# Performance work log

Measured on AMD Instinct MI355X. Metric: run time of the kernel, lower is better.

The kernel has to match this reference:

```python
import jax, jax.numpy as jnp
import numpy as np

DECAY = 0.95     # importance_decay
BUDGET = 1.0     # attention_budget
TOP_K = 10       # recall top_k used by get_context_embedding
EPS = 1e-8


def _gelu(x):
    # torch nn.GELU default = exact erf variant
    return jax.nn.gelu(x, approximate=False)


def setup_inputs() -> dict:
    key = jax.random.key(0)
    ks = jax.random.split(key, 8)
    B, N, D, H = 4096, 100, 4096, 128
    query = jax.random.normal(ks[0], (B, D), dtype=jnp.float32)
    seg_emb = jax.random.normal(ks[1], (N, D), dtype=jnp.float32)
    positions = jnp.arange(N, dtype=jnp.int32)
    s1 = 1.0 / np.sqrt(D)
    s2 = 1.0 / np.sqrt(H)
    iw1 = jax.random.normal(ks[2], (D, H), dtype=jnp.float32) * s1
    ib1 = jnp.zeros((H,), dtype=jnp.float32)
    iw2 = jax.random.normal(ks[3], (H, 1), dtype=jnp.float32) * s2
    ib2 = jnp.zeros((1,), dtype=jnp.float32)
    rw1 = jax.random.normal(ks[4], (2 * D, H), dtype=jnp.float32) * (1.0 / np.sqrt(2 * D))
    rb1 = jnp.zeros((H,), dtype=jnp.float32)
    rw2 = jax.random.normal(ks[5], (H, 1), dtype=jnp.float32) * s2
    rb2 = jnp.zeros((1,), dtype=jnp.float32)
    return {"query": query, "seg_emb": seg_emb, "positions": positions,
            "iw1": iw1, "ib1": ib1, "iw2": iw2, "ib2": ib2,
            "rw1": rw1, "rb1": rb1, "rw2": rw2, "rb2": rb2}


def reference(query, seg_emb, positions, iw1, ib1, iw2, ib2, rw1, rb1, rw2, rb2):
    # query: [B, D], seg_emb: [N, D]
    B, D = query.shape
    N = seg_emb.shape[0]

    # importance_scorer per segment: Linear->GELU->Linear->Sigmoid, [N]
    importance = jax.nn.sigmoid(_gelu(seg_emb @ iw1 + ib1) @ iw2 + ib2)[:, 0]

    # relevance_scorer on concat([query, seg]); split rw1 to avoid [B,N,2D] concat
    qh = query @ rw1[:D]            # [B, H]
    sh = seg_emb @ rw1[D:]          # [N, H]
    h = _gelu(qh[:, None, :] + sh[None, :, :] + rb1)   # [B, N, H]
    rel = jax.nn.sigmoid(jnp.einsum('bnh,ho->bn', h, rw2) + rb2[0])  # [B, N]

    # recall score: importance * relevance * (0.5 + 0.5 * decay^(N - pos - 1))
    pos_factor = DECAY ** (N - positions.astype(jnp.float32) - 1.0)  # [N]
    score = importance[None, :] * rel * (0.5 + 0.5 * pos_factor[None, :])

    _, topi = jax.lax.top_k(score, TOP_K)               # [B, K]

    sel_rel = jnp.take_along_axis(rel, topi, axis=1)    # [B, K]
    sel_imp = importance[topi]                          # [B, K]
    w = sel_imp * sel_rel
    w = w / (jnp.sum(w, axis=-1, keepdims=True) + EPS) * BUDGET

    sel_emb = seg_emb[topi]                             # [B, K, D]
    context = jnp.einsum('bk,bkd->bd', w, sel_emb)      # [B, D]
    return query + context
```

## Files before the change

kernel.cpp:

```cpp
#include <hip/hip_runtime.h>
#include <math.h>

#define DDIM 4096
#define NSEG 100
#define HDIM 128
#define BROWS 4096
#define TOPK 10
#define KSLICES 8

typedef __attribute__((ext_vector_type(8))) short bf16x8;
typedef __attribute__((ext_vector_type(4))) float f32x4;
typedef __attribute__((ext_vector_type(2))) float f32x2;

__device__ __forceinline__ void gl16(const void* g, void* l) {
    __builtin_amdgcn_global_load_lds(
        (const __attribute__((address_space(1))) unsigned int*)g,
        (__attribute__((address_space(3))) unsigned int*)l,
        16, 0, 0);
}

__device__ __forceinline__ float gelu_f(float x) {
    float u  = x * 0.70710678118654752440f;
    float au = fminf(fabsf(u), 3.9f);
    float t  = __builtin_amdgcn_rcpf(fmaf(0.3275911f, au, 1.0f));
    float p  = fmaf(fmaf(fmaf(fmaf(1.061405429f, t, -1.453152027f), t,
                              1.421413741f), t, -0.284496736f), t, 0.254829592f) * t;
    float e  = __expf(-au * au);
    float er = fmaf(-p, e, 1.0f);
    er = copysignf(er, u);
    return 0.5f * x * (1.0f + er);
}

__device__ __forceinline__ f32x2 gelu2(f32x2 x) {
    f32x2 u  = x * 0.70710678118654752440f;
    f32x2 au = __builtin_elementwise_min(__builtin_elementwise_abs(u), (f32x2)(3.9f));
    f32x2 den = __builtin_elementwise_fma((f32x2)(0.3275911f), au, (f32x2)(1.0f));
    f32x2 t;
    t.x = __builtin_amdgcn_rcpf(den.x);
    t.y = __builtin_amdgcn_rcpf(den.y);
    f32x2 p = __builtin_elementwise_fma(
                __builtin_elementwise_fma(
                  __builtin_elementwise_fma(
                    __builtin_elementwise_fma((f32x2)(1.061405429f), t, (f32x2)(-1.453152027f)),
                    t, (f32x2)(1.421413741f)),
                  t, (f32x2)(-0.284496736f)),
                t, (f32x2)(0.254829592f)) * t;
    f32x2 e;
    e.x = __expf(-au.x * au.x);
    e.y = __expf(-au.y * au.y);
    f32x2 er = __builtin_elementwise_fma(-p, e, (f32x2)(1.0f));
    er.x = copysignf(er.x, u.x);
    er.y = copysignf(er.y, u.y);
    return 0.5f * x * ((f32x2)(1.0f) + er);
}

__device__ __forceinline__ void split8(const float4& a, const float4& b,
                                       bf16x8& hi, bf16x8& lo) {
    float v[8] = {a.x, a.y, a.z, a.w, b.x, b.y, b.z, b.w};
    uint hw[4], lw[4];
    #pragma unroll
    for (int j = 0; j < 4; ++j) {
        uint u0 = __float_as_uint(v[2 * j]);
        uint u1 = __float_as_uint(v[2 * j + 1]);
        hw[j] = (u0 >> 16) | (u1 & 0xffff0000u);
        float r0 = v[2 * j]     - __uint_as_float(u0 & 0xffff0000u);
        float r1 = v[2 * j + 1] - __uint_as_float(u1 & 0xffff0000u);
        lw[j] = (__float_as_uint(r0) >> 16) | (__float_as_uint(r1) & 0xffff0000u);
    }
    uint4 h = make_uint4(hw[0], hw[1], hw[2], hw[3]);
    uint4 l = make_uint4(lw[0], lw[1], lw[2], lw[3]);
    hi = __builtin_bit_cast(bf16x8, h);
    lo = __builtin_bit_cast(bf16x8, l);
}

__global__ void k_front(const float* __restrict__ seg,
                        const float* __restrict__ iw1,
                        const float* __restrict__ rw1,
                        float* __restrict__ segp,
                        unsigned char* __restrict__ btI) {
    __shared__ __align__(16) float shf[32 * 129];
    int bid = blockIdx.x, tid = threadIdx.x;
    if (bid < 1600) {
        float (*segT)[5] = reinterpret_cast<float (*)[5]>(shf);
        int ng = bid % 25;
        int ks = (bid / 25) * 64;
        {
            int k = tid & 63, j = tid >> 6;
            segT[k][j] = seg[(size_t)(ng * 4 + j) * DDIM + ks + k];
        }
        __syncthreads();
        int col = tid;
        float a0 = 0.f, a1 = 0.f, a2 = 0.f, a3 = 0.f;
        const float* w = (col < HDIM) ? (iw1 + col)
                                      : (rw1 + (size_t)DDIM * HDIM + (col - HDIM));
        #pragma unroll 8
        for (int k = 0; k < 64; ++k) {
            float wv = w[(size_t)(ks + k) * HDIM];
            a0 = fmaf(segT[k][0], wv, a0);
            a1 = fmaf(segT[k][1], wv, a1);
            a2 = fmaf(segT[k][2], wv, a2);
            a3 = fmaf(segT[k][3], wv, a3);
        }
        float* outp = segp + (size_t)(bid / 25) * (NSEG * 256) + (size_t)(ng * 4) * 256 + col;
        outp[0] = a0; outp[256] = a1; outp[512] = a2; outp[768] = a3;
    } else {
        float (*tile)[129] = reinterpret_cast<float (*)[129]>(shf);
        int c = bid - 1600;
        #pragma unroll
        for (int i = 0; i < 4; ++i) {
            int e = i * 1024 + tid * 4;
            int k = e >> 7, n = e & 127;
            *reinterpret_cast<float4*>(&tile[k][n]) =
                *reinterpret_cast<const float4*>(rw1 + (size_t)(c * 32 + k) * HDIM + n);
        }
        __syncthreads();
        unsigned char* img = btI + (size_t)c * 16384;
        #pragma unroll
        for (int uu = 0; uu < 2; ++uu) {
            int U = tid * 2 + uu;
            int col = U >> 2;
            int u = U & 3;
            int Z = (col * 64 + u * 16) ^ ((col & 7) << 4);
            uint hw[4], lw[4];
            #pragma unroll
            for (int j = 0; j < 4; ++j) {
                float x0 = tile[u * 8 + 2 * j][col];
                float x1 = tile[u * 8 + 2 * j + 1][col];
                uint u0 = __float_as_uint(x0), u1 = __float_as_uint(x1);
                hw[j] = (u0 >> 16) | (u1 & 0xffff0000u);
                float r0 = x0 - __uint_as_float(u0 & 0xffff0000u);
                float r1 = x1 - __uint_as_float(u1 & 0xffff0000u);
                lw[j] = (__float_as_uint(r0) >> 16) | (__float_as_uint(r1) & 0xffff0000u);
            }
            *reinterpret_cast<uint4*>(img + Z)        = make_uint4(hw[0], hw[1], hw[2], hw[3]);
            *reinterpret_cast<uint4*>(img + 8192 + Z) = make_uint4(lw[0], lw[1], lw[2], lw[3]);
        }
    }
}

__global__ __launch_bounds__(256)
void k_mid(const float* __restrict__ query,
           const unsigned char* __restrict__ btI,
           float* __restrict__ qhp,
           const float* __restrict__ segp,
           const int* __restrict__ positions,
           const float* __restrict__ ib1,
           const float* __restrict__ iw2,
           const float* __restrict__ ib2,
           const float* __restrict__ rb1,
           float* __restrict__ shwT, float* __restrict__ impA,
           float* __restrict__ cA) {
    __shared__ __align__(16) char lds[49152];
    int bid = blockIdx.x, tid = threadIdx.x;
    if (bid < 512) {
        float  (*Ab)[2048] = reinterpret_cast<float (*)[2048]>(lds);
        ushort (*Bb)[8192] = reinterpret_cast<ushort (*)[8192]>(lds + 16384);
        int lane = tid & 63, w = tid >> 6;
        int cl = lane & 15, rg = lane >> 4;
        int wm = w >> 1, wn = w & 1;
        int m0 = (bid & 63) * 64;
        int ky = bid >> 6;
        int k0 = ky * 512;

        const float* aSrc0;
        const float* aSrc1;
        {
            int X0 = w * 2048 + lane * 16;
            int r0_ = X0 >> 7, kb0 = (X0 & 127) ^ ((r0_ & 7) << 4);
            aSrc0 = query + (size_t)(m0 + r0_) * DDIM + k0 + (kb0 >> 2);
            int X1 = X0 + 1024;
            int r1_ = X1 >> 7, kb1 = (X1 & 127) ^ ((r1_ & 7) << 4);
            aSrc1 = query + (size_t)(m0 + r1_) * DDIM + k0 + (kb1 >> 2);
        }
        const unsigned char* bSrc = btI + (size_t)(ky * 16) * 16384 + w * 4096 + lane * 16;

        f32x4 acc[2][4];
        #pragma unroll
        for (int mi = 0; mi < 2; ++mi)
            #pragma unroll
            for (int nf = 0; nf < 4; ++nf) acc[mi][nf] = (f32x4)0.f;

        {
            char* ad = (char*)&Ab[0][0] + w * 2048;
            char* bd = (char*)&Bb[0][0] + w * 4096;
            gl16(aSrc0, ad);
            gl16(aSrc1, ad + 1024);
            #pragma unroll
            for (int j = 0; j < 4; ++j) gl16(bSrc + j * 1024, bd + j * 1024);
        }
        __syncthreads();

        #pragma unroll 2
        for (int t = 0; t < 16; ++t) {
            int cur = t & 1;
            if (t < 15) {
                char* ad = (char*)&Ab[cur ^ 1][0] + w * 2048;
                char* bd = (char*)&Bb[cur ^ 1][0] + w * 4096;
                gl16(aSrc0 + (t + 1) * 32, ad);
                gl16(aSrc1 + (t + 1) * 32, ad + 1024);
                const unsigned char* bs = bSrc + (size_t)(t + 1) * 16384;
                #pragma unroll
                for (int j = 0; j < 4; ++j) gl16(bs + j * 1024, bd + j * 1024);
            }
            bf16x8 ah[2], al[2];
            #pragma unroll
            for (int mi = 0; mi < 2; ++mi) {
                int row = wm * 32 + mi * 16 + cl;
                int sw = (row & 7) << 4;
                int Sb = row * 128 + rg * 32;
                float4 f0 = *reinterpret_cast<const float4*>((const char*)&Ab[cur][0] + (Sb ^ sw));
                float4 f1 = *reinterpret_cast<const float4*>((const char*)&Ab[cur][0] + ((Sb + 16) ^ sw));
                split8(f0, f1, ah[mi], al[mi]);
            }
            #pragma unroll
            for (int nf = 0; nf < 4; ++nf) {
                int col = wn * 64 + nf * 16 + cl;
                int Z = (col * 64 + rg * 16) ^ ((col & 7) << 4);
                bf16x8 bh = *reinterpret_cast<const bf16x8*>((const char*)&Bb[cur][0] + Z);
                bf16x8 bl = *reinterpret_cast<const bf16x8*>((const char*)&Bb[cur][0] + 8192 + Z);
                #pragma unroll
                for (int mi = 0; mi < 2; ++mi) {
                    acc[mi][nf] = __builtin_amdgcn_mfma_f32_16x16x32_bf16(ah[mi], bh, acc[mi][nf], 0, 0, 0);
                    acc[mi][nf] = __builtin_amdgcn_mfma_f32_16x16x32_bf16(al[mi], bh, acc[mi][nf], 0, 0, 0);
                    acc[mi][nf] = __builtin_amdgcn_mfma_f32_16x16x32_bf16(ah[mi], bl, acc[mi][nf], 0, 0, 0);
                }
            }
            __syncthreads();
        }

        float* op = qhp + (size_t)ky * (BROWS * HDIM);
        #pragma unroll
        for (int mi = 0; mi < 2; ++mi) {
            int rowb = m0 + wm * 32 + mi * 16 + rg * 4;
            #pragma unroll
            for (int nf = 0; nf < 4; ++nf) {
                int col = wn * 64 + nf * 16 + cl;
                #pragma unroll
                for (int r = 0; r < 4; ++r)
                    op[(size_t)(rowb + r) * HDIM + col] = acc[mi][nf][r];
            }
        }
    } else {
        float* red = reinterpret_cast<float*>(lds);
        int n = bid - 512;
        float v = 0.f;
        #pragma unroll
        for (int s = 0; s < 64; ++s)
            v += segp[(size_t)s * (NSEG * 256) + (size_t)n * 256 + tid];
        if (tid < HDIM) {
            red[tid] = gelu_f(v + ib1[tid]) * iw2[tid];
        } else {
            shwT[(size_t)(tid - HDIM) * NSEG + n] = v + rb1[tid - HDIM];
        }
        __syncthreads();
        if (tid == 0) {
            float s = 0.f;
            for (int j = 0; j < HDIM; ++j) s += red[j];
            float imp = 1.f / (1.f + expf(-(s + ib2[0])));
            float pf = powf(0.95f, (float)NSEG - (float)positions[n] - 1.0f);
            impA[n] = imp;
            cA[n] = imp * (0.5f + 0.5f * pf);
        }
    }
}

__global__ __launch_bounds__(256)
void k_rel(const float* __restrict__ qhp,
           const float* __restrict__ shwT,
           const float* __restrict__ rw2,
           const float* __restrict__ rb2,
           const float* __restrict__ impA,
           const float* __restrict__ cA,
           int* __restrict__ idxA,
           float* __restrict__ wnA) {
    __shared__ float qs[4][HDIM];
    __shared__ float scL[4][128], wiL[4][128];
    int tid = threadIdx.x;
    int b0 = blockIdx.x * 4;

    #pragma unroll
    for (int i = 0; i < 2; ++i) {
        int idx = tid + i * 256;
        int r = idx >> 7, h = idx & 127;
        size_t o = (size_t)(b0 + r) * HDIM + h;
        float v = qhp[o];
        #pragma unroll
        for (int s = 1; s < KSLICES; ++s)
            v += qhp[(size_t)s * (BROWS * HDIM) + o];
        qs[r][h] = v;
    }
    __syncthreads();

    int w = tid >> 6, lane = tid & 63;
    int r = w;
    bool act = (lane < 50);
    int n0 = act ? (2 * lane) : 98;
    f32x2 a0_ = (f32x2)(0.f), a1_ = (f32x2)(0.f);
    f32x2 a2_ = (f32x2)(0.f), a3_ = (f32x2)(0.f);
    #pragma unroll 2
    for (int h = 0; h < 32; ++h) {
        f32x2 sA = *reinterpret_cast<const f32x2*>(&shwT[(h)      * NSEG + n0]);
        f32x2 sB = *reinterpret_cast<const f32x2*>(&shwT[(h + 32) * NSEG + n0]);
        f32x2 sC = *reinterpret_cast<const f32x2*>(&shwT[(h + 64) * NSEG + n0]);
        f32x2 sD = *reinterpret_cast<const f32x2*>(&shwT[(h + 96) * NSEG + n0]);
        a0_ = __builtin_elementwise_fma(gelu2(qs[r][h]      + sA), (f32x2)(rw2[h]),      a0_);
        a1_ = __builtin_elementwise_fma(gelu2(qs[r][h + 32] + sB), (f32x2)(rw2[h + 32]), a1_);
        a2_ = __builtin_elementwise_fma(gelu2(qs[r][h + 64] + sC), (f32x2)(rw2[h + 64]), a2_);
        a3_ = __builtin_elementwise_fma(gelu2(qs[r][h + 96] + sD), (f32x2)(rw2[h + 96]), a3_);
    }
    f32x2 acc = (a0_ + a1_) + (a2_ + a3_);
    if (act) {
        float rb2f = rb2[0];
        float rel0 = 1.f / (1.f + expf(-(acc.x + rb2f)));
        float rel1 = 1.f / (1.f + expf(-(acc.y + rb2f)));
        scL[r][n0]     = cA[n0] * rel0;      wiL[r][n0]     = impA[n0] * rel0;
        scL[r][n0 + 1] = cA[n0 + 1] * rel1;  wiL[r][n0 + 1] = impA[n0 + 1] * rel1;
    }
    __syncthreads();

    {
        int rr = w;
        float s1 = scL[rr][lane];
        float w1 = wiL[rr][lane];
        int i2 = lane + 64;
        float s2 = (i2 < NSEG) ? scL[rr][i2] : -1e30f;
        float w2 = (i2 < NSEG) ? wiL[rr][i2] : 0.f;

        float wv[TOPK]; int idxv[TOPK]; float wsum = 0.f;
        #pragma unroll
        for (int k = 0; k < TOPK; ++k) {
            float s; int i;
            if (s2 > s1) { s = s2; i = i2; } else { s = s1; i = lane; }
            #pragma unroll
            for (int off = 1; off < 64; off <<= 1) {
                float os = __shfl_xor(s, off);
                int oi = __shfl_xor(i, off);
                if (os > s || (os == s && oi < i)) { s = os; i = oi; }
            }
            float wi = __shfl((i < 64) ? w1 : w2, i & 63);
            idxv[k] = i; wv[k] = wi; wsum += wi;
            if (i == lane) s1 = -1e30f;
            if (i == i2)   s2 = -1e30f;
        }
        if (lane == 0) {
            int b = b0 + rr;
            float denom = wsum + 1e-8f;
            #pragma unroll
            for (int k = 0; k < TOPK; ++k) {
                idxA[b * TOPK + k] = idxv[k];
                wnA[b * TOPK + k]  = wv[k] / denom;
            }
        }
    }
}

__global__ void k_gather(const float* __restrict__ query,
                         const float* __restrict__ seg,
                         const int* __restrict__ idxA,
                         const float* __restrict__ wnA,
                         float* __restrict__ out) {
    int b = blockIdx.x, tid = threadIdx.x;
    const int*   ip = idxA + b * TOPK;
    const float* wp = wnA  + b * TOPK;
    float wn[TOPK]; const float* srow[TOPK];
    #pragma unroll
    for (int k = 0; k < TOPK; ++k) {
        wn[k]   = wp[k];
        srow[k] = seg + (size_t)ip[k] * DDIM;
    }
    const float* qrow = query + (size_t)b * DDIM;
    float* orow = out + (size_t)b * DDIM;

    float4 q[4];
    #pragma unroll
    for (int c = 0; c < 4; ++c)
        q[c] = *reinterpret_cast<const float4*>(qrow + c * 1024 + tid * 4);
    #pragma unroll
    for (int k = 0; k < TOPK; ++k) {
        float4 s[4];
        #pragma unroll
        for (int c = 0; c < 4; ++c)
            s[c] = *reinterpret_cast<const float4*>(srow[k] + c * 1024 + tid * 4);
        #pragma unroll
        for (int c = 0; c < 4; ++c) {
            q[c].x = fmaf(wn[k], s[c].x, q[c].x);
            q[c].y = fmaf(wn[k], s[c].y, q[c].y);
            q[c].z = fmaf(wn[k], s[c].z, q[c].z);
            q[c].w = fmaf(wn[k], s[c].w, q[c].w);
        }
    }
    #pragma unroll
    for (int c = 0; c < 4; ++c) {
        f32x4 v = __builtin_bit_cast(f32x4, q[c]);
        __builtin_nontemporal_store(v, reinterpret_cast<f32x4*>(orow + c * 1024 + tid * 4));
    }
}

extern "C" void kernel_launch(void* const* d_in, const int* in_sizes, int n_in,
                              void* d_out, int out_size, void* d_ws, size_t ws_size,
                              hipStream_t stream) {
    const float* query = (const float*)d_in[0];
    const float* seg   = (const float*)d_in[1];
    const int*   pos   = (const int*)d_in[2];
    const float* iw1   = (const float*)d_in[3];
    const float* ib1   = (const float*)d_in[4];
    const float* iw2   = (const float*)d_in[5];
    const float* ib2   = (const float*)d_in[6];
    const float* rw1   = (const float*)d_in[7];
    const float* rb1   = (const float*)d_in[8];
    const float* rw2   = (const float*)d_in[9];
    const float* rb2   = (const float*)d_in[10];
    float* out = (float*)d_out;

    char* ws = (char*)d_ws;
    float* qhp  = (float*)(ws);
    float* segp = (float*)(ws + 16 * 1024 * 1024);
    unsigned char* btI = (unsigned char*)(ws + 23 * 1024 * 1024);
    float* shwT = (float*)(ws + 25 * 1024 * 1024);
    float* impA = (float*)(ws + 25 * 1024 * 1024 + 64 * 1024);
    float* cA   = (float*)(ws + 25 * 1024 * 1024 + 64 * 1024 + 4096);
    int*   idxA = (int*)  (ws + 25 * 1024 * 1024 + 128 * 1024);
    float* wnA  = (float*)(ws + 25 * 1024 * 1024 + 320 * 1024);

    hipLaunchKernelGGL(k_front, dim3(1728), dim3(256), 0, stream,
                       seg, iw1, rw1, segp, btI);
    hipLaunchKernelGGL(k_mid, dim3(612), dim3(256), 0, stream,
                       query, btI, qhp, segp, pos, ib1, iw2, ib2, rb1,
                       shwT, impA, cA);
    hipLaunchKernelGGL(k_rel, dim3(BROWS / 4), dim3(256), 0, stream,
                       qhp, shwT, rw2, rb2, impA, cA, idxA, wnA);
    hipLaunchKernelGGL(k_gather, dim3(BROWS), dim3(256), 0, stream,
                       query, seg, idxA, wnA, out);
}
```

Measured before the change: 111.4 us.

## Replace top-k gather with dense sparse-weight GEMM on MFMA using split bf16

Instead of storing top-k indices and weights and gathering ten segment rows per query row, k_rel now writes a dense [B,128] weight row (zeros outside the selected segments) split into hi/lo bf16 parts. A new k_wgemm multiplies this weight matrix by a pre-packed, swizzled bf16 hi/lo image of seg_emb (built in extra k_front blocks) using MFMA with three products per tile, then adds query. This turns irregular gathered reads into a dense tensor-core GEMM with double-buffered LDS loads. It adds conversion work and a small precision change from the three-term bf16 split.

```diff
diff --git a/kernel.cpp b/kernel.cpp
--- a/kernel.cpp
+++ b/kernel.cpp
@@ -77,7 +77,8 @@
                         const float* __restrict__ iw1,
                         const float* __restrict__ rw1,
                         float* __restrict__ segp,
-                        unsigned char* __restrict__ btI) {
+                        unsigned char* __restrict__ btI,
+                        unsigned char* __restrict__ segI) {
     __shared__ __align__(16) float shf[32 * 129];
     int bid = blockIdx.x, tid = threadIdx.x;
     if (bid < 1600) {
@@ -103,7 +104,7 @@
         }
         float* outp = segp + (size_t)(bid / 25) * (NSEG * 256) + (size_t)(ng * 4) * 256 + col;
         outp[0] = a0; outp[256] = a1; outp[512] = a2; outp[768] = a3;
-    } else {
+    } else if (bid < 1728) {
         float (*tile)[129] = reinterpret_cast<float (*)[129]>(shf);
         int c = bid - 1600;
         #pragma unroll
@@ -115,6 +116,42 @@
         }
         __syncthreads();
         unsigned char* img = btI + (size_t)c * 16384;
+        #pragma unroll
+        for (int uu = 0; uu < 2; ++uu) {
+            int U = tid * 2 + uu;
+            int col = U >> 2;
+            int u = U & 3;
+            int Z = (col * 64 + u * 16) ^ ((col & 7) << 4);
+            uint hw[4], lw[4];
+            #pragma unroll
+            for (int j = 0; j < 4; ++j) {
+                float x0 = tile[u * 8 + 2 * j][col];
+                float x1 = tile[u * 8 + 2 * j + 1][col];
+                uint u0 = __float_as_uint(x0), u1 = __float_as_uint(x1);
+                hw[j] = (u0 >> 16) | (u1 & 0xffff0000u);
+                float r0 = x0 - __uint_as_float(u0 & 0xffff0000u);
+                float r1 = x1 - __uint_as_float(u1 & 0xffff0000u);
+                lw[j] = (__float_as_uint(r0) >> 16) | (__float_as_uint(r1) & 0xffff0000u);
+            }
+            *reinterpret_cast<uint4*>(img + Z)        = make_uint4(hw[0], hw[1], hw[2], hw[3]);
+            *reinterpret_cast<uint4*>(img + 8192 + Z) = make_uint4(lw[0], lw[1], lw[2], lw[3]);
+        }
+    } else {
+        float (*tile)[129] = reinterpret_cast<float (*)[129]>(shf);
+        int c2 = bid - 1728;
+        int db = c2 >> 2, ks = c2 & 3;
+        #pragma unroll
+        for (int i = 0; i < 4; ++i) {
+            int e = i * 1024 + tid * 4;
+            int k = e >> 7, n = e & 127;
+            int gk = ks * 32 + k;
+            float4 v = (gk < NSEG)
+                ? *reinterpret_cast<const float4*>(seg + (size_t)gk * DDIM + db * 128 + n)
+                : make_float4(0.f, 0.f, 0.f, 0.f);
+            *reinterpret_cast<float4*>(&tile[k][n]) = v;
+        }
+        __syncthreads();
+        unsigned char* img = segI + (size_t)c2 * 16384;
         #pragma unroll
         for (int uu = 0; uu < 2; ++uu) {
             int U = tid * 2 + uu;
@@ -271,8 +308,8 @@
            const float* __restrict__ rb2,
            const float* __restrict__ impA,
            const float* __restrict__ cA,
-           int* __restrict__ idxA,
-           float* __restrict__ wnA) {
+           ushort* __restrict__ Wh,
+           ushort* __restrict__ Wl) {
     __shared__ float qs[4][HDIM];
     __shared__ float scL[4][128], wiL[4][128];
     int tid = threadIdx.x;
@@ -342,57 +379,101 @@
             if (i == lane) s1 = -1e30f;
             if (i == i2)   s2 = -1e30f;
         }
-        if (lane == 0) {
-            int b = b0 + rr;
-            float denom = wsum + 1e-8f;
-            #pragma unroll
-            for (int k = 0; k < TOPK; ++k) {
-                idxA[b * TOPK + k] = idxv[k];
-                wnA[b * TOPK + k]  = wv[k] / denom;
-            }
-        }
-    }
-}
-
-__global__ void k_gather(const float* __restrict__ query,
-                         const float* __restrict__ seg,
-                         const int* __restrict__ idxA,
-                         const float* __restrict__ wnA,
-                         float* __restrict__ out) {
-    int b = blockIdx.x, tid = threadIdx.x;
-    const int*   ip = idxA + b * TOPK;
-    const float* wp = wnA  + b * TOPK;
-    float wn[TOPK]; const float* srow[TOPK];
+        int b = b0 + rr;
+        float inv = 1.0f / (wsum + 1e-8f);
+        int c0 = 2 * lane, c1 = c0 + 1;
+        float w0 = 0.f, w1d = 0.f;
+        #pragma unroll
+        for (int k = 0; k < TOPK; ++k) {
+            float wk = wv[k] * inv;
+            if (idxv[k] == c0) w0  = wk;
+            if (idxv[k] == c1) w1d = wk;
+        }
+        uint u0 = __float_as_uint(w0), u1 = __float_as_uint(w1d);
+        uint h01 = (u0 >> 16) | (u1 & 0xffff0000u);
+        float r0 = w0  - __uint_as_float(u0 & 0xffff0000u);
+        float r1 = w1d - __uint_as_float(u1 & 0xffff0000u);
+        uint l01 = (__float_as_uint(r0) >> 16) | (__float_as_uint(r1) & 0xffff0000u);
+        reinterpret_cast<uint*>(Wh)[b * 64 + lane] = h01;
+        reinterpret_cast<uint*>(Wl)[b * 64 + lane] = l01;
+    }
+}
+
+__global__ __launch_bounds__(256)
+void k_wgemm(const float* __restrict__ query,
+             const ushort* __restrict__ Wh,
+             const ushort* __restrict__ Wl,
+             const unsigned char* __restrict__ segI,
+             float* __restrict__ out) {
+    __shared__ __align__(16) ushort Bb[2][8192];
+    int tid = threadIdx.x;
+    int lane = tid & 63, w = tid >> 6;
+    int cl = lane & 15, rg = lane >> 4;
+    int wm = w >> 1, wn = w & 1;
+    int m0 = blockIdx.x * 64;
+    int d0 = blockIdx.y * 128;
+
+    const unsigned char* bSrc = segI + (size_t)(blockIdx.y * 4) * 16384 + w * 4096 + lane * 16;
+
+    f32x4 acc[2][4];
     #pragma unroll
-    for (int k = 0; k < TOPK; ++k) {
-        wn[k]   = wp[k];
-        srow[k] = seg + (size_t)ip[k] * DDIM;
-    }
-    const float* qrow = query + (size_t)b * DDIM;
-    float* orow = out + (size_t)b * DDIM;
-
-    float4 q[4];
+    for (int mi = 0; mi < 2; ++mi)
+        #pragma unroll
+        for (int nf = 0; nf < 4; ++nf) acc[mi][nf] = (f32x4)0.f;
+
+    {
+        char* bd = (char*)&Bb[0][0] + w * 4096;
+        #pragma unroll
+        for (int j = 0; j < 4; ++j) gl16(bSrc + j * 1024, bd + j * 1024);
+    }
+    __syncthreads();
+
     #pragma unroll
-    for (int c = 0; c < 4; ++c)
-        q[c] = *reinterpret_cast<const float4*>(qrow + c * 1024 + tid * 4);
+    for (int t = 0; t < 4; ++t) {
+        int cur = t & 1;
+        if (t < 3) {
+            char* bd = (char*)&Bb[cur ^ 1][0] + w * 4096;
+            const unsigned char* bs = bSrc + (size_t)(t + 1) * 16384;
+            #pragma unroll
+            for (int j = 0; j < 4; ++j) gl16(bs + j * 1024, bd + j * 1024);
+        }
+        bf16x8 ah[2], al[2];
+        #pragma unroll
+        for (int mi = 0; mi < 2; ++mi) {
+            int row = m0 + wm * 32 + mi * 16 + cl;
+            size_t ao = (size_t)row * HDIM + t * 32 + rg * 8;
+            ah[mi] = *reinterpret_cast<const bf16x8*>(Wh + ao);
+            al[mi] = *reinterpret_cast<const bf16x8*>(Wl + ao);
+        }
+        #pragma unroll
+        for (int nf = 0; nf < 4; ++nf) {
+            int col = wn * 64 + nf * 16 + cl;
+            int Z = (col * 64 + rg * 16) ^ ((col & 7) << 4);
+            bf16x8 bh = *reinterpret_cast<const bf16x8*>((const char*)&Bb[cur][0] + Z);
+            bf16x8 bl = *reinterpret_cast<const bf16x8*>((const char*)&Bb[cur][0] + 8192 + Z);
+            #pragma unroll
+            for (int mi = 0; mi < 2; ++mi) {
+                acc[mi][nf] = __builtin_amdgcn_mfma_f32_16x16x32_bf16(ah[mi], bh, acc[mi][nf], 0, 0, 0);
+                acc[mi][nf] = __builtin_amdgcn_mfma_f32_16x16x32_bf16(al[mi], bh, acc[mi][nf], 0, 0, 0);
+                acc[mi][nf] = __builtin_amdgcn_mfma_f32_16x16x32_bf16(ah[mi], bl, acc[mi][nf], 0, 0, 0);
+            }
+        }
+        __syncthreads();
+    }
+
     #pragma unroll
-    for (int k = 0; k < TOPK; ++k) {
-        float4 s[4];
-        #pragma unroll
-        for (int c = 0; c < 4; ++c)
-            s[c] = *reinterpret_cast<const float4*>(srow[k] + c * 1024 + tid * 4);
-        #pragma unroll
-        for (int c = 0; c < 4; ++c) {
-            q[c].x = fmaf(wn[k], s[c].x, q[c].x);
-            q[c].y = fmaf(wn[k], s[c].y, q[c].y);
-            q[c].z = fmaf(wn[k], s[c].z, q[c].z);
-            q[c].w = fmaf(wn[k], s[c].w, q[c].w);
-        }
-    }
-    #pragma unroll
-    for (int c = 0; c < 4; ++c) {
-        f32x4 v = __builtin_bit_cast(f32x4, q[c]);
-        __builtin_nontemporal_store(v, reinterpret_cast<f32x4*>(orow + c * 1024 + tid * 4));
+    for (int mi = 0; mi < 2; ++mi) {
+        int rowb = m0 + wm * 32 + mi * 16 + rg * 4;
+        #pragma unroll
+        for (int nf = 0; nf < 4; ++nf) {
+            int col = d0 + wn * 64 + nf * 16 + cl;
+            #pragma unroll
+            for (int r = 0; r < 4; ++r) {
+                size_t o = (size_t)(rowb + r) * DDIM + col;
+                float v = query[o] + acc[mi][nf][r];
+                __builtin_nontemporal_store(v, out + o);
+            }
+        }
     }
 }
 
@@ -415,20 +496,21 @@
     char* ws = (char*)d_ws;
     float* qhp  = (float*)(ws);
     float* segp = (float*)(ws + 16 * 1024 * 1024);
-    unsigned char* btI = (unsigned char*)(ws + 23 * 1024 * 1024);
-    float* shwT = (float*)(ws + 25 * 1024 * 1024);
-    float* impA = (float*)(ws + 25 * 1024 * 1024 + 64 * 1024);
-    float* cA   = (float*)(ws + 25 * 1024 * 1024 + 64 * 1024 + 4096);
-    int*   idxA = (int*)  (ws + 25 * 1024 * 1024 + 128 * 1024);
-    float* wnA  = (float*)(ws + 25 * 1024 * 1024 + 320 * 1024);
-
-    hipLaunchKernelGGL(k_front, dim3(1728), dim3(256), 0, stream,
-                       seg, iw1, rw1, segp, btI);
+    unsigned char* btI  = (unsigned char*)(ws + 23 * 1024 * 1024);
+    unsigned char* segI = (unsigned char*)(ws + 25 * 1024 * 1024);
+    float* shwT = (float*)(ws + 27 * 1024 * 1024);
+    float* impA = (float*)(ws + 27 * 1024 * 1024 + 64 * 1024);
+    float* cA   = (float*)(ws + 27 * 1024 * 1024 + 64 * 1024 + 4096);
+    ushort* Wh  = (ushort*)(ws + 28 * 1024 * 1024);
+    ushort* Wl  = (ushort*)(ws + 29 * 1024 * 1024);
+
+    hipLaunchKernelGGL(k_front, dim3(1856), dim3(256), 0, stream,
+                       seg, iw1, rw1, segp, btI, segI);
     hipLaunchKernelGGL(k_mid, dim3(612), dim3(256), 0, stream,
                        query, btI, qhp, segp, pos, ib1, iw2, ib2, rb1,
                        shwT, impA, cA);
     hipLaunchKernelGGL(k_rel, dim3(BROWS / 4), dim3(256), 0, stream,
-                       qhp, shwT, rw2, rb2, impA, cA, idxA, wnA);
-    hipLaunchKernelGGL(k_gather, dim3(BROWS), dim3(256), 0, stream,
-                       query, seg, idxA, wnA, out);
-}
+                       qhp, shwT, rw2, rb2, impA, cA, Wh, Wl);
+    hipLaunchKernelGGL(k_wgemm, dim3(64, 32), dim3(256), 0, stream,
+                       query, Wh, Wl, segI, out);
+}
```

Measured after the change: 122.3 us. +9.8%, slower.

## Double-buffer gathered segment rows through LDS with async global-to-LDS loads

Applied to the files above, without the earlier changes.

Rewrites the final gather/accumulate kernel so the ten selected segment rows are staged chunk by chunk into a double-buffered shared-memory tile using direct global-to-LDS loads. Each of the eight chunks is processed with float2 accesses while the next chunk's load is in flight. The goal is to overlap the segment-row fetch latency with the FMA accumulation and query read. In exchange it adds a block barrier per chunk, 40 KB of LDS per block (which can lower occupancy), and narrower per-thread global accesses for query and output.

```diff
diff --git a/kernel.cpp b/kernel.cpp
--- a/kernel.cpp
+++ b/kernel.cpp
@@ -354,12 +354,15 @@
     }
 }
 
-__global__ void k_gather(const float* __restrict__ query,
-                         const float* __restrict__ seg,
-                         const int* __restrict__ idxA,
-                         const float* __restrict__ wnA,
-                         float* __restrict__ out) {
+__global__ __launch_bounds__(256)
+void k_gather(const float* __restrict__ query,
+              const float* __restrict__ seg,
+              const int* __restrict__ idxA,
+              const float* __restrict__ wnA,
+              float* __restrict__ out) {
+    __shared__ __align__(16) float sbuf[2][20 * 256];
     int b = blockIdx.x, tid = threadIdx.x;
+    int lane = tid & 63, w = tid >> 6;
     const int*   ip = idxA + b * TOPK;
     const float* wp = wnA  + b * TOPK;
     float wn[TOPK]; const float* srow[TOPK];
@@ -371,29 +374,34 @@
     const float* qrow = query + (size_t)b * DDIM;
     float* orow = out + (size_t)b * DDIM;
 
-    float4 q[4];
+    #define STAGE(c, buf)                                                        \
+        _Pragma("unroll")                                                        \
+        for (int j = 0; j < 5; ++j) {                                            \
+            int m = w * 5 + j;                                                   \
+            gl16(srow[m >> 1] + (c) * 512 + (m & 1) * 256 + lane * 4,            \
+                 (char*)&sbuf[buf][0] + m * 1024);                               \
+        }
+
+    STAGE(0, 0)
+    __syncthreads();
+
     #pragma unroll
-    for (int c = 0; c < 4; ++c)
-        q[c] = *reinterpret_cast<const float4*>(qrow + c * 1024 + tid * 4);
-    #pragma unroll
-    for (int k = 0; k < TOPK; ++k) {
-        float4 s[4];
-        #pragma unroll
-        for (int c = 0; c < 4; ++c)
-            s[c] = *reinterpret_cast<const float4*>(srow[k] + c * 1024 + tid * 4);
-        #pragma unroll
-        for (int c = 0; c < 4; ++c) {
-            q[c].x = fmaf(wn[k], s[c].x, q[c].x);
-            q[c].y = fmaf(wn[k], s[c].y, q[c].y);
-            q[c].z = fmaf(wn[k], s[c].z, q[c].z);
-            q[c].w = fmaf(wn[k], s[c].w, q[c].w);
-        }
-    }
-    #pragma unroll
-    for (int c = 0; c < 4; ++c) {
-        f32x4 v = __builtin_bit_cast(f32x4, q[c]);
-        __builtin_nontemporal_store(v, reinterpret_cast<f32x4*>(orow + c * 1024 + tid * 4));
-    }
+    for (int c = 0; c < 8; ++c) {
+        int buf = c & 1;
+        if (c < 7) { STAGE(c + 1, buf ^ 1) }
+        float2 q2 = *reinterpret_cast<const float2*>(qrow + c * 512 + tid * 2);
+        const float2* s2 = reinterpret_cast<const float2*>(&sbuf[buf][0]);
+        #pragma unroll
+        for (int k = 0; k < TOPK; ++k) {
+            float2 sv = s2[k * 256 + tid];
+            q2.x = fmaf(wn[k], sv.x, q2.x);
+            q2.y = fmaf(wn[k], sv.y, q2.y);
+        }
+        f32x2 v; v.x = q2.x; v.y = q2.y;
+        __builtin_nontemporal_store(v, reinterpret_cast<f32x2*>(orow + c * 512 + tid * 2));
+        __syncthreads();
+    }
+    #undef STAGE
 }
 
 extern "C" void kernel_launch(void* const* d_in, const int* in_sizes, int n_in,
```

New measurement: 117.5 us. +5.5%, slower.
